# Optimization experiments

Measured on AMD Instinct MI355X. Metric: run time of the kernel, lower is better.

## Reference

```python
import jax, jax.numpy as jnp
import numpy as np

B, NQ, NK = 8, 1024, 1024
DQ = DK = DV = 512
H = 8
DH = DV // H
EPS = 1e-5
NEG = -1e9


def _layer_norm(x, g, b):
    mu = jnp.mean(x, axis=-1, keepdims=True)
    var = jnp.mean(jnp.square(x - mu), axis=-1, keepdims=True)
    return (x - mu) * jax.lax.rsqrt(var + EPS) * g + b


def setup_inputs() -> dict:
    key = jax.random.key(0)
    ks = jax.random.split(key, 16)
    s_q = 1.0 / np.sqrt(DQ)
    s_k = 1.0 / np.sqrt(DK)
    s_v = 1.0 / np.sqrt(DV)
    return {
        "Q": jax.random.normal(ks[0], (B, NQ, DQ), jnp.float32),
        "K": jax.random.normal(ks[1], (B, NK, DK), jnp.float32),
        "mask": jax.random.randint(ks[2], (B, NK), 0, 2, jnp.int32),
        "Wq": jax.random.uniform(ks[3], (DQ, DV), jnp.float32, -s_q, s_q),
        "bq": jax.random.uniform(ks[4], (DV,), jnp.float32, -s_q, s_q),
        "Wk": jax.random.uniform(ks[5], (DK, DV), jnp.float32, -s_k, s_k),
        "bk": jax.random.uniform(ks[6], (DV,), jnp.float32, -s_k, s_k),
        "Wv": jax.random.uniform(ks[7], (DK, DV), jnp.float32, -s_k, s_k),
        "bv": jax.random.uniform(ks[8], (DV,), jnp.float32, -s_k, s_k),
        "Wo": jax.random.uniform(ks[9], (DV, DV), jnp.float32, -s_v, s_v),
        "bo": jax.random.uniform(ks[10], (DV,), jnp.float32, -s_v, s_v),
        "g0": jnp.ones((DV,), jnp.float32),
        "b0": jnp.zeros((DV,), jnp.float32),
        "g1": jnp.ones((DV,), jnp.float32),
        "b1": jnp.zeros((DV,), jnp.float32),
    }


def reference(Q, K, mask, Wq, bq, Wk, bk, Wv, bv, Wo, bo, g0, b0, g1, b1):
    b = Q.shape[0]
    # projections: [B, N, DV] -> [B, N, H, DH]
    q = (Q @ Wq + bq).reshape(b, -1, H, DH)
    k = (K @ Wk + bk).reshape(b, -1, H, DH)
    v = (K @ Wv + bv).reshape(b, -1, H, DH)
    scores = jnp.einsum("bqhd,bkhd->bhqk", q, k) / np.sqrt(DH)  # [B,H,Nq,Nk]
    scores = jnp.where((mask == 0)[:, None, None, :], NEG, scores)
    A = jax.nn.softmax(scores, axis=-1)
    o = q + jnp.einsum("bhqk,bkhd->bqhd", A, v)  # residual on projected Q (per head)
    O = o.reshape(b, -1, DV)
    O = _layer_norm(O, g0, b0)
    O = O + jax.nn.relu(O @ Wo + bo)
    O = _layer_norm(O, g1, b1)
    return O
```

## Files before the change

### kernel.cpp

```cpp
#include <hip/hip_runtime.h>


typedef float f32x4 __attribute__((ext_vector_type(4)));
typedef short bf16x8 __attribute__((ext_vector_type(8)));
typedef unsigned short u16;

#define MFMA16 __builtin_amdgcn_mfma_f32_16x16x32_bf16

__device__ __forceinline__ float bf2f(u16 u){
    unsigned x = ((unsigned)u) << 16;
    return __builtin_bit_cast(float, x);
}
__device__ __forceinline__ u16 f2bf(float f){
    unsigned u = __builtin_bit_cast(unsigned, f);
    u = u + 0x7fffu + ((u >> 16) & 1u);
    return (u16)(u >> 16);
}

__global__ __launch_bounds__(256) void transpose_w(
    const float* __restrict__ Wq, const float* __restrict__ Wk,
    const float* __restrict__ Wv, const float* __restrict__ Wo,
    u16* __restrict__ wt)
{
    const int z = blockIdx.z;
    const float* W = (z == 0) ? Wq : (z == 1) ? Wk : (z == 2) ? Wv : Wo;
    u16* out = wt + (size_t)z * 512 * 512;

    __shared__ u16 tile[32][33];
    const int k0 = blockIdx.y * 32, n0 = blockIdx.x * 32;
    const int c = threadIdx.x & 31, r = threadIdx.x >> 5;
#pragma unroll
    for (int i = 0; i < 4; i++) {
        int rr = r + i * 8;
        tile[rr][c] = f2bf(W[(size_t)(k0 + rr) * 512 + n0 + c]);
    }
    __syncthreads();
#pragma unroll
    for (int i = 0; i < 4; i++) {
        int rr = r + i * 8;
        out[(size_t)(n0 + rr) * 512 + k0 + c] = tile[c][rr];
    }
}

__global__ __launch_bounds__(256) void transpose_v(
    const u16* __restrict__ vb, u16* __restrict__ vtg)
{
    __shared__ u16 tile[32][33];
    const int bh = blockIdx.z;
    const int b = bh >> 3, h = bh & 7;
    const int k0 = blockIdx.x * 32, d0 = blockIdx.y * 32;
    const int c = threadIdx.x & 31, r = threadIdx.x >> 5;
#pragma unroll
    for (int i = 0; i < 4; i++) {
        int rr = r + i * 8;
        tile[rr][c] = vb[(size_t)(b * 1024 + k0 + rr) * 512 + h * 64 + d0 + c];
    }
    __syncthreads();
#pragma unroll
    for (int i = 0; i < 4; i++) {
        int rr = r + i * 8;
        vtg[(size_t)(bh * 64 + d0 + rr) * 1024 + k0 + c] = tile[c][rr];
    }
}

__global__ __launch_bounds__(256) void gemm_proj(
    const float* __restrict__ Q, const float* __restrict__ K,
    const u16* __restrict__ wt,
    const float* __restrict__ bq, const float* __restrict__ bk, const float* __restrict__ bv,
    u16* __restrict__ qb, u16* __restrict__ kb, u16* __restrict__ vb)
{
    __shared__ __align__(16) u16 lds_a[128 * 40];
    __shared__ __align__(16) u16 lds_b[128 * 40];

    const int z = blockIdx.z;
    const float* X = (z == 0) ? Q : K;
    const u16* Wt = wt + (size_t)z * 512 * 512;
    const float* bias = (z == 0) ? bq : (z == 1) ? bk : bv;
    u16* outb = (z == 0) ? qb : (z == 1) ? kb : vb;

    const int bm = blockIdx.y, bn = blockIdx.x;
    const int t = threadIdx.x;
    const int wave = t >> 6, lane = t & 63, quad = lane >> 4, lm = lane & 15;
    const int wm = wave >> 1, wn = wave & 1;

    f32x4 acc[4][4];
    const f32x4 zz = {0.f, 0.f, 0.f, 0.f};
#pragma unroll
    for (int i = 0; i < 4; i++)
#pragma unroll
        for (int j = 0; j < 4; j++) acc[i][j] = zz;

    for (int k0 = 0; k0 < 512; k0 += 32) {
#pragma unroll
        for (int i = 0; i < 2; i++) {
            int idx = t + i * 256;
            int r = idx >> 2, c = (idx & 3) * 8;
            const float* xp = &X[(size_t)(bm * 128 + r) * 512 + k0 + c];
            f32x4 a0 = *(const f32x4*)xp;
            f32x4 a1 = *(const f32x4*)(xp + 4);
            bf16x8 xv;
#pragma unroll
            for (int j = 0; j < 4; j++) { xv[j] = (short)f2bf(a0[j]); xv[4 + j] = (short)f2bf(a1[j]); }
            *(bf16x8*)&lds_a[r * 40 + c] = xv;
            *(bf16x8*)&lds_b[r * 40 + c] =
                *(const bf16x8*)&Wt[(size_t)(bn * 128 + r) * 512 + k0 + c];
        }
        __syncthreads();
        bf16x8 af[4], bfr[4];
#pragma unroll
        for (int mi = 0; mi < 4; mi++)
            af[mi] = *(const bf16x8*)&lds_a[(wm * 64 + mi * 16 + lm) * 40 + quad * 8];
#pragma unroll
        for (int ni = 0; ni < 4; ni++)
            bfr[ni] = *(const bf16x8*)&lds_b[(wn * 64 + ni * 16 + lm) * 40 + quad * 8];
#pragma unroll
        for (int mi = 0; mi < 4; mi++)
#pragma unroll
            for (int ni = 0; ni < 4; ni++)
                acc[mi][ni] = MFMA16(af[mi], bfr[ni], acc[mi][ni], 0, 0, 0);
        __syncthreads();
    }

#pragma unroll
    for (int mi = 0; mi < 4; mi++) {
#pragma unroll
        for (int ni = 0; ni < 4; ni++) {
            const int col = bn * 128 + wn * 64 + ni * 16 + lm;
            const float bv_ = bias[col];
#pragma unroll
            for (int r = 0; r < 4; r++) {
                const int row = bm * 128 + wm * 64 + mi * 16 + quad * 4 + r;
                outb[(size_t)row * 512 + col] = f2bf(acc[mi][ni][r] + bv_);
            }
        }
    }
}

__global__ __launch_bounds__(256) void gemm_mlp(
    const u16* __restrict__ X, const u16* __restrict__ wt,
    const float* __restrict__ bo, const float* __restrict__ resid,
    float* __restrict__ outf)
{
    __shared__ __align__(16) u16 lds_a[128 * 40];
    __shared__ __align__(16) u16 lds_b[128 * 40];

    const u16* Wt = wt + (size_t)3 * 512 * 512;
    const int bm = blockIdx.y, bn = blockIdx.x;
    const int t = threadIdx.x;
    const int wave = t >> 6, lane = t & 63, quad = lane >> 4, lm = lane & 15;
    const int wm = wave >> 1, wn = wave & 1;

    f32x4 acc[4][4];
    const f32x4 zz = {0.f, 0.f, 0.f, 0.f};
#pragma unroll
    for (int i = 0; i < 4; i++)
#pragma unroll
        for (int j = 0; j < 4; j++) acc[i][j] = zz;

    for (int k0 = 0; k0 < 512; k0 += 32) {
#pragma unroll
        for (int i = 0; i < 2; i++) {
            int idx = t + i * 256;
            int r = idx >> 2, c = (idx & 3) * 8;
            *(bf16x8*)&lds_a[r * 40 + c] =
                *(const bf16x8*)&X[(size_t)(bm * 128 + r) * 512 + k0 + c];
            *(bf16x8*)&lds_b[r * 40 + c] =
                *(const bf16x8*)&Wt[(size_t)(bn * 128 + r) * 512 + k0 + c];
        }
        __syncthreads();
        bf16x8 af[4], bfr[4];
#pragma unroll
        for (int mi = 0; mi < 4; mi++)
            af[mi] = *(const bf16x8*)&lds_a[(wm * 64 + mi * 16 + lm) * 40 + quad * 8];
#pragma unroll
        for (int ni = 0; ni < 4; ni++)
            bfr[ni] = *(const bf16x8*)&lds_b[(wn * 64 + ni * 16 + lm) * 40 + quad * 8];
#pragma unroll
        for (int mi = 0; mi < 4; mi++)
#pragma unroll
            for (int ni = 0; ni < 4; ni++)
                acc[mi][ni] = MFMA16(af[mi], bfr[ni], acc[mi][ni], 0, 0, 0);
        __syncthreads();
    }

#pragma unroll
    for (int mi = 0; mi < 4; mi++) {
#pragma unroll
        for (int ni = 0; ni < 4; ni++) {
            const int col = bn * 128 + wn * 64 + ni * 16 + lm;
            const float bv_ = bo[col];
#pragma unroll
            for (int r = 0; r < 4; r++) {
                const int row = bm * 128 + wm * 64 + mi * 16 + quad * 4 + r;
                const size_t off = (size_t)row * 512 + col;
                outf[off] = resid[off] + fmaxf(acc[mi][ni][r] + bv_, 0.f);
            }
        }
    }
}

__global__ __launch_bounds__(256, 4) void attn_kernel(
    const u16* __restrict__ qb, const u16* __restrict__ kb, const u16* __restrict__ vtg,
    const int* __restrict__ mask, float* __restrict__ O)
{
    __shared__ __align__(16) u16 k_tile[64 * 88];
    __shared__ __align__(16) u16 vt[64 * 88];
    __shared__ __align__(16) u16 p_st[4 * 16 * 88];
    __shared__ float mbias[1024];

    const int i = blockIdx.x;
    const int s_ = i >> 3;
    const int bh = (i & 7) + 8 * (s_ >> 4);
    const int qt = s_ & 15;
    const int b = bh >> 3, h = bh & 7;

    const int t = threadIdx.x, wave = t >> 6, lane = t & 63;
    const int quad = lane >> 4, lm = lane & 15;
    const int qbase = qt * 64 + wave * 16;
    const size_t baseb = (size_t)b * 1024 * 512;
    const size_t vbase = (size_t)((b * 8 + h) * 64) * 1024;

#pragma unroll
    for (int ii = 0; ii < 4; ii++) {
        int j = t + ii * 256;
        mbias[j] = mask[b * 1024 + j] ? 0.0f : -30000.0f;
    }

    bf16x8 aq[2];
#pragma unroll
    for (int ks = 0; ks < 2; ks++)
        aq[ks] = *(const bf16x8*)&qb[baseb +
            (size_t)(qbase + lm) * 512 + h * 64 + ks * 32 + quad * 8];

    float lsum[4] = {0.f, 0.f, 0.f, 0.f};
    f32x4 oacc[4];
    const f32x4 zz = {0.f, 0.f, 0.f, 0.f};
#pragma unroll
    for (int c = 0; c < 4; c++) oacc[c] = zz;

    const float SC2 = 0.125f * 1.44269504088896341f;
    const int srow = t >> 2, scol = (t & 3) * 16;
    u16* pw = &p_st[wave * 16 * 88];

    const u16* kgp = &kb[baseb + (size_t)srow * 512 + h * 64 + scol];
    const u16* vgp = &vtg[vbase + (size_t)srow * 1024 + scol];

    bf16x8 kA0, kA1, vA0, vA1, kB0, kB1, vB0, vB1;

    auto load_t = [&](int kt, bf16x8& k0, bf16x8& k1, bf16x8& v0, bf16x8& v1) {
        const u16* kp = kgp + (size_t)kt * 64 * 512;
        k0 = *(const bf16x8*)kp;
        k1 = *(const bf16x8*)(kp + 8);
        const u16* vp = vgp + kt * 64;
        v0 = *(const bf16x8*)vp;
        v1 = *(const bf16x8*)(vp + 8);
    };
    auto store_t = [&](bf16x8 k0, bf16x8 k1, bf16x8 v0, bf16x8 v1) {
        *(bf16x8*)&k_tile[srow * 88 + scol]     = k0;
        *(bf16x8*)&k_tile[srow * 88 + scol + 8] = k1;
        *(bf16x8*)&vt[srow * 88 + scol]     = v0;
        *(bf16x8*)&vt[srow * 88 + scol + 8] = v1;
    };

    auto compute_t = [&](int kt) {
        const int keyg = kt * 64;
        bf16x8 bk[4][2];
#pragma unroll
        for (int n = 0; n < 4; n++)
#pragma unroll
            for (int ks = 0; ks < 2; ks++)
                bk[n][ks] = *(const bf16x8*)&k_tile[(n * 16 + lm) * 88 + ks * 32 + quad * 8];

#pragma unroll
        for (int n = 0; n < 4; n++) {
            f32x4 S = zz;
            __builtin_amdgcn_s_setprio(1);
            S = MFMA16(aq[0], bk[n][0], S, 0, 0, 0);
            S = MFMA16(aq[1], bk[n][1], S, 0, 0, 0);
            __builtin_amdgcn_s_setprio(0);
            const float bias = mbias[keyg + n * 16 + lm];
#pragma unroll
            for (int r = 0; r < 4; r++) {
                float p = __builtin_amdgcn_exp2f(__builtin_fmaf(S[r], SC2, bias));
                lsum[r] += p;
                pw[(quad * 4 + r) * 88 + n * 16 + lm] = f2bf(p);
            }
        }

#pragma unroll
        for (int ks = 0; ks < 2; ks++) {
            bf16x8 ap = *(const bf16x8*)&pw[lm * 88 + ks * 32 + quad * 8];
            __builtin_amdgcn_s_setprio(1);
#pragma unroll
            for (int c = 0; c < 4; c++) {
                bf16x8 bv_ = *(const bf16x8*)&vt[(c * 16 + lm) * 88 + ks * 32 + quad * 8];
                oacc[c] = MFMA16(ap, bv_, oacc[c], 0, 0, 0);
            }
            __builtin_amdgcn_s_setprio(0);
        }
    };

    load_t(0, kA0, kA1, vA0, vA1);

    for (int kt = 0; kt < 16; kt += 2) {
        store_t(kA0, kA1, vA0, vA1);
        load_t(kt + 1, kB0, kB1, vB0, vB1);
        __syncthreads();
        compute_t(kt);
        __syncthreads();
        store_t(kB0, kB1, vB0, vB1);
        load_t((kt + 2) & 15, kA0, kA1, vA0, vA1);
        __syncthreads();
        compute_t(kt + 1);
        __syncthreads();
    }

#pragma unroll
    for (int r = 0; r < 4; r++) {
        float s = lsum[r];
        s += __shfl_xor(s, 1); s += __shfl_xor(s, 2);
        s += __shfl_xor(s, 4); s += __shfl_xor(s, 8);
        lsum[r] = s;
    }

#pragma unroll
    for (int c = 0; c < 4; c++)
#pragma unroll
        for (int r = 0; r < 4; r++) {
            const int row = qbase + quad * 4 + r;
            const int d = h * 64 + c * 16 + lm;
            const size_t off = baseb + (size_t)row * 512 + d;
            O[off] = bf2f(qb[off]) + oacc[c][r] / lsum[r];
        }
}

__global__ __launch_bounds__(256) void ln_kernel(
    const float* __restrict__ in, const float* __restrict__ g, const float* __restrict__ bsh,
    u16* __restrict__ outb, float* __restrict__ outf)
{
    const int row = blockIdx.x * 4 + (threadIdx.x >> 6);
    const int lane = threadIdx.x & 63;
    const float* x = in + (size_t)row * 512 + lane * 8;
    float v[8];
    *(f32x4*)&v[0] = *(const f32x4*)&x[0];
    *(f32x4*)&v[4] = *(const f32x4*)&x[4];
    float s = 0.f, sq = 0.f;
#pragma unroll
    for (int j = 0; j < 8; j++) { s += v[j]; sq += v[j] * v[j]; }
#pragma unroll
    for (int off = 1; off < 64; off <<= 1) {
        s += __shfl_xor(s, off);
        sq += __shfl_xor(sq, off);
    }
    const float mu = s * (1.f / 512.f);
    const float var = sq * (1.f / 512.f) - mu * mu;
    const float rs = rsqrtf(var + 1e-5f);
    float y[8];
#pragma unroll
    for (int j = 0; j < 8; j++) {
        int col = lane * 8 + j;
        y[j] = (v[j] - mu) * rs * g[col] + bsh[col];
    }
    if (outb != nullptr) {
        bf16x8 ov;
#pragma unroll
        for (int j = 0; j < 8; j++) ov[j] = (short)f2bf(y[j]);
        *(bf16x8*)&outb[(size_t)row * 512 + lane * 8] = ov;
    }
    if (outf != nullptr) {
        float* o = outf + (size_t)row * 512 + lane * 8;
        *(f32x4*)&o[0] = *(const f32x4*)&y[0];
        *(f32x4*)&o[4] = *(const f32x4*)&y[4];
    }
}

extern "C" void kernel_launch(void* const* d_in, const int* in_sizes, int n_in,
                              void* d_out, int out_size, void* d_ws, size_t ws_size,
                              hipStream_t stream) {
    const float* Q  = (const float*)d_in[0];
    const float* K  = (const float*)d_in[1];
    const int* mask = (const int*)d_in[2];
    const float* Wq = (const float*)d_in[3];
    const float* bq = (const float*)d_in[4];
    const float* Wk = (const float*)d_in[5];
    const float* bk = (const float*)d_in[6];
    const float* Wv = (const float*)d_in[7];
    const float* bv = (const float*)d_in[8];
    const float* Wo = (const float*)d_in[9];
    const float* bo = (const float*)d_in[10];
    const float* g0 = (const float*)d_in[11];
    const float* b0 = (const float*)d_in[12];
    const float* g1 = (const float*)d_in[13];
    const float* b1 = (const float*)d_in[14];
    float* out = (float*)d_out;

    char* ws = (char*)d_ws;
    const size_t MB = 1048576;
    u16*   wt  = (u16*)(ws);
    u16*   qb  = (u16*)(ws + 2 * MB);
    u16*   kb  = (u16*)(ws + 10 * MB);
    u16*   vtg = (u16*)(ws + 18 * MB);
    u16*   vb  = (u16*)(ws + 26 * MB);
    float* Of  = (float*)(ws + 26 * MB);
    u16*   O1b = (u16*)(ws + 2 * MB);
    float* O1f = (float*)(ws + 10 * MB);
    float* Uf  = (float*)(ws + 26 * MB);

    transpose_w<<<dim3(16, 16, 4), 256, 0, stream>>>(Wq, Wk, Wv, Wo, wt);
    gemm_proj<<<dim3(4, 64, 3), 256, 0, stream>>>(Q, K, wt, bq, bk, bv, qb, kb, vb);
    transpose_v<<<dim3(32, 2, 64), 256, 0, stream>>>(vb, vtg);
    attn_kernel<<<1024, 256, 0, stream>>>(qb, kb, vtg, mask, Of);
    ln_kernel<<<2048, 256, 0, stream>>>(Of, g0, b0, O1b, O1f);
    gemm_mlp<<<dim3(4, 64, 1), 256, 0, stream>>>(O1b, wt, bo, O1f, Uf);
    ln_kernel<<<2048, 256, 0, stream>>>(Uf, g1, b1, nullptr, out);
}
```

Before: 207.4 us.

## Fuse V transpose into projection epilogue, pre-convert inputs, drop mask LDS staging

The V projection epilogue now writes its result straight into the per-head transposed layout, which removes the separate transpose_v kernel and its round trip through global memory. Q and K are converted to bf16 once in a new convert_x kernel, so the projection GEMM loads bf16 tiles instead of converting fp32 inside its inner loop. The attention kernel stops staging a mask-bias array in LDS and instead reads the mask from global memory on each key tile. In exchange this adds an extra kernel and extra bf16 buffers in the workspace, and the mask reads become repeated global loads.

```diff
diff --git a/kernel.cpp b/kernel.cpp
--- a/kernel.cpp
+++ b/kernel.cpp
@@ -4,6 +4,7 @@
 typedef float f32x4 __attribute__((ext_vector_type(4)));
 typedef short bf16x8 __attribute__((ext_vector_type(8)));
 typedef unsigned short u16;
+typedef unsigned short u16x4 __attribute__((ext_vector_type(4)));
 
 #define MFMA16 __builtin_amdgcn_mfma_f32_16x16x32_bf16
 
@@ -42,109 +43,36 @@
     }
 }
 
-__global__ __launch_bounds__(256) void transpose_v(
-    const u16* __restrict__ vb, u16* __restrict__ vtg)
-{
-    __shared__ u16 tile[32][33];
-    const int bh = blockIdx.z;
-    const int b = bh >> 3, h = bh & 7;
-    const int k0 = blockIdx.x * 32, d0 = blockIdx.y * 32;
-    const int c = threadIdx.x & 31, r = threadIdx.x >> 5;
-#pragma unroll
-    for (int i = 0; i < 4; i++) {
-        int rr = r + i * 8;
-        tile[rr][c] = vb[(size_t)(b * 1024 + k0 + rr) * 512 + h * 64 + d0 + c];
-    }
-    __syncthreads();
-#pragma unroll
-    for (int i = 0; i < 4; i++) {
-        int rr = r + i * 8;
-        vtg[(size_t)(bh * 64 + d0 + rr) * 1024 + k0 + c] = tile[c][rr];
-    }
+__global__ __launch_bounds__(256) void convert_x(
+    const float* __restrict__ Q, const float* __restrict__ K,
+    u16* __restrict__ xq, u16* __restrict__ xk)
+{
+    const float* src = blockIdx.y ? K : Q;
+    u16* dst = blockIdx.y ? xk : xq;
+    const size_t i = ((size_t)blockIdx.x * 256 + threadIdx.x) * 8;
+    f32x4 a0 = *(const f32x4*)&src[i];
+    f32x4 a1 = *(const f32x4*)&src[i + 4];
+    bf16x8 v;
+#pragma unroll
+    for (int j = 0; j < 4; j++) { v[j] = (short)f2bf(a0[j]); v[4 + j] = (short)f2bf(a1[j]); }
+    *(bf16x8*)&dst[i] = v;
 }
 
 __global__ __launch_bounds__(256) void gemm_proj(
-    const float* __restrict__ Q, const float* __restrict__ K,
+    const u16* __restrict__ xq, const u16* __restrict__ xk,
     const u16* __restrict__ wt,
     const float* __restrict__ bq, const float* __restrict__ bk, const float* __restrict__ bv,
-    u16* __restrict__ qb, u16* __restrict__ kb, u16* __restrict__ vb)
+    u16* __restrict__ qb, u16* __restrict__ kb, u16* __restrict__ vtg)
 {
     __shared__ __align__(16) u16 lds_a[128 * 40];
     __shared__ __align__(16) u16 lds_b[128 * 40];
 
     const int z = blockIdx.z;
-    const float* X = (z == 0) ? Q : K;
+    const u16* X = (z == 0) ? xq : xk;
     const u16* Wt = wt + (size_t)z * 512 * 512;
     const float* bias = (z == 0) ? bq : (z == 1) ? bk : bv;
-    u16* outb = (z == 0) ? qb : (z == 1) ? kb : vb;
-
-    const int bm = blockIdx.y, bn = blockIdx.x;
-    const int t = threadIdx.x;
-    const int wave = t >> 6, lane = t & 63, quad = lane >> 4, lm = lane & 15;
-    const int wm = wave >> 1, wn = wave & 1;
-
-    f32x4 acc[4][4];
-    const f32x4 zz = {0.f, 0.f, 0.f, 0.f};
-#pragma unroll
-    for (int i = 0; i < 4; i++)
-#pragma unroll
-        for (int j = 0; j < 4; j++) acc[i][j] = zz;
-
-    for (int k0 = 0; k0 < 512; k0 += 32) {
-#pragma unroll
-        for (int i = 0; i < 2; i++) {
-            int idx = t + i * 256;
-            int r = idx >> 2, c = (idx & 3) * 8;
-            const float* xp = &X[(size_t)(bm * 128 + r) * 512 + k0 + c];
-            f32x4 a0 = *(const f32x4*)xp;
-            f32x4 a1 = *(const f32x4*)(xp + 4);
-            bf16x8 xv;
-#pragma unroll
-            for (int j = 0; j < 4; j++) { xv[j] = (short)f2bf(a0[j]); xv[4 + j] = (short)f2bf(a1[j]); }
-            *(bf16x8*)&lds_a[r * 40 + c] = xv;
-            *(bf16x8*)&lds_b[r * 40 + c] =
-                *(const bf16x8*)&Wt[(size_t)(bn * 128 + r) * 512 + k0 + c];
-        }
-        __syncthreads();
-        bf16x8 af[4], bfr[4];
-#pragma unroll
-        for (int mi = 0; mi < 4; mi++)
-            af[mi] = *(const bf16x8*)&lds_a[(wm * 64 + mi * 16 + lm) * 40 + quad * 8];
-#pragma unroll
-        for (int ni = 0; ni < 4; ni++)
-            bfr[ni] = *(const bf16x8*)&lds_b[(wn * 64 + ni * 16 + lm) * 40 + quad * 8];
-#pragma unroll
-        for (int mi = 0; mi < 4; mi++)
-#pragma unroll
-            for (int ni = 0; ni < 4; ni++)
-                acc[mi][ni] = MFMA16(af[mi], bfr[ni], acc[mi][ni], 0, 0, 0);
-        __syncthreads();
-    }
-
-#pragma unroll
-    for (int mi = 0; mi < 4; mi++) {
-#pragma unroll
-        for (int ni = 0; ni < 4; ni++) {
-            const int col = bn * 128 + wn * 64 + ni * 16 + lm;
-            const float bv_ = bias[col];
-#pragma unroll
-            for (int r = 0; r < 4; r++) {
-                const int row = bm * 128 + wm * 64 + mi * 16 + quad * 4 + r;
-                outb[(size_t)row * 512 + col] = f2bf(acc[mi][ni][r] + bv_);
-            }
-        }
-    }
-}
-
-__global__ __launch_bounds__(256) void gemm_mlp(
-    const u16* __restrict__ X, const u16* __restrict__ wt,
-    const float* __restrict__ bo, const float* __restrict__ resid,
-    float* __restrict__ outf)
-{
-    __shared__ __align__(16) u16 lds_a[128 * 40];
-    __shared__ __align__(16) u16 lds_b[128 * 40];
-
-    const u16* Wt = wt + (size_t)3 * 512 * 512;
+    u16* outb = (z == 0) ? qb : kb;
+
     const int bm = blockIdx.y, bn = blockIdx.x;
     const int t = threadIdx.x;
     const int wave = t >> 6, lane = t & 63, quad = lane >> 4, lm = lane & 15;
@@ -183,6 +111,86 @@
         __syncthreads();
     }
 
+    if (z == 2) {
+#pragma unroll
+        for (int mi = 0; mi < 4; mi++) {
+            const int key0 = bm * 128 + wm * 64 + mi * 16 + quad * 4;
+            const int bb = key0 >> 10, key = key0 & 1023;
+#pragma unroll
+            for (int ni = 0; ni < 4; ni++) {
+                const int col = bn * 128 + wn * 64 + ni * 16 + lm;
+                const float bv_ = bias[col];
+                const int hh = col >> 6, dd = col & 63;
+                u16x4 pk;
+#pragma unroll
+                for (int r = 0; r < 4; r++) pk[r] = f2bf(acc[mi][ni][r] + bv_);
+                *(u16x4*)&vtg[((size_t)((bb * 8 + hh) * 64 + dd)) * 1024 + key] = pk;
+            }
+        }
+    } else {
+#pragma unroll
+        for (int mi = 0; mi < 4; mi++) {
+#pragma unroll
+            for (int ni = 0; ni < 4; ni++) {
+                const int col = bn * 128 + wn * 64 + ni * 16 + lm;
+                const float bv_ = bias[col];
+#pragma unroll
+                for (int r = 0; r < 4; r++) {
+                    const int row = bm * 128 + wm * 64 + mi * 16 + quad * 4 + r;
+                    outb[(size_t)row * 512 + col] = f2bf(acc[mi][ni][r] + bv_);
+                }
+            }
+        }
+    }
+}
+
+__global__ __launch_bounds__(256) void gemm_mlp(
+    const u16* __restrict__ X, const u16* __restrict__ wt,
+    const float* __restrict__ bo, const float* __restrict__ resid,
+    float* __restrict__ outf)
+{
+    __shared__ __align__(16) u16 lds_a[128 * 40];
+    __shared__ __align__(16) u16 lds_b[128 * 40];
+
+    const u16* Wt = wt + (size_t)3 * 512 * 512;
+    const int bm = blockIdx.y, bn = blockIdx.x;
+    const int t = threadIdx.x;
+    const int wave = t >> 6, lane = t & 63, quad = lane >> 4, lm = lane & 15;
+    const int wm = wave >> 1, wn = wave & 1;
+
+    f32x4 acc[4][4];
+    const f32x4 zz = {0.f, 0.f, 0.f, 0.f};
+#pragma unroll
+    for (int i = 0; i < 4; i++)
+#pragma unroll
+        for (int j = 0; j < 4; j++) acc[i][j] = zz;
+
+    for (int k0 = 0; k0 < 512; k0 += 32) {
+#pragma unroll
+        for (int i = 0; i < 2; i++) {
+            int idx = t + i * 256;
+            int r = idx >> 2, c = (idx & 3) * 8;
+            *(bf16x8*)&lds_a[r * 40 + c] =
+                *(const bf16x8*)&X[(size_t)(bm * 128 + r) * 512 + k0 + c];
+            *(bf16x8*)&lds_b[r * 40 + c] =
+                *(const bf16x8*)&Wt[(size_t)(bn * 128 + r) * 512 + k0 + c];
+        }
+        __syncthreads();
+        bf16x8 af[4], bfr[4];
+#pragma unroll
+        for (int mi = 0; mi < 4; mi++)
+            af[mi] = *(const bf16x8*)&lds_a[(wm * 64 + mi * 16 + lm) * 40 + quad * 8];
+#pragma unroll
+        for (int ni = 0; ni < 4; ni++)
+            bfr[ni] = *(const bf16x8*)&lds_b[(wn * 64 + ni * 16 + lm) * 40 + quad * 8];
+#pragma unroll
+        for (int mi = 0; mi < 4; mi++)
+#pragma unroll
+            for (int ni = 0; ni < 4; ni++)
+                acc[mi][ni] = MFMA16(af[mi], bfr[ni], acc[mi][ni], 0, 0, 0);
+        __syncthreads();
+    }
+
 #pragma unroll
     for (int mi = 0; mi < 4; mi++) {
 #pragma unroll
@@ -206,7 +214,6 @@
     __shared__ __align__(16) u16 k_tile[64 * 88];
     __shared__ __align__(16) u16 vt[64 * 88];
     __shared__ __align__(16) u16 p_st[4 * 16 * 88];
-    __shared__ float mbias[1024];
 
     const int i = blockIdx.x;
     const int s_ = i >> 3;
@@ -219,12 +226,7 @@
     const int qbase = qt * 64 + wave * 16;
     const size_t baseb = (size_t)b * 1024 * 512;
     const size_t vbase = (size_t)((b * 8 + h) * 64) * 1024;
-
-#pragma unroll
-    for (int ii = 0; ii < 4; ii++) {
-        int j = t + ii * 256;
-        mbias[j] = mask[b * 1024 + j] ? 0.0f : -30000.0f;
-    }
+    const int* mrow = &mask[b * 1024];
 
     bf16x8 aq[2];
 #pragma unroll
@@ -264,6 +266,11 @@
 
     auto compute_t = [&](int kt) {
         const int keyg = kt * 64;
+        float bias_n[4];
+#pragma unroll
+        for (int n = 0; n < 4; n++)
+            bias_n[n] = mrow[keyg + n * 16 + lm] ? 0.0f : -30000.0f;
+
         bf16x8 bk[4][2];
 #pragma unroll
         for (int n = 0; n < 4; n++)
@@ -278,10 +285,9 @@
             S = MFMA16(aq[0], bk[n][0], S, 0, 0, 0);
             S = MFMA16(aq[1], bk[n][1], S, 0, 0, 0);
             __builtin_amdgcn_s_setprio(0);
-            const float bias = mbias[keyg + n * 16 + lm];
 #pragma unroll
             for (int r = 0; r < 4; r++) {
-                float p = __builtin_amdgcn_exp2f(__builtin_fmaf(S[r], SC2, bias));
+                float p = __builtin_amdgcn_exp2f(__builtin_fmaf(S[r], SC2, bias_n[n]));
                 lsum[r] += p;
                 pw[(quad * 4 + r) * 88 + n * 16 + lm] = f2bf(p);
             }
@@ -400,15 +406,16 @@
     u16*   qb  = (u16*)(ws + 2 * MB);
     u16*   kb  = (u16*)(ws + 10 * MB);
     u16*   vtg = (u16*)(ws + 18 * MB);
-    u16*   vb  = (u16*)(ws + 26 * MB);
+    u16*   xq  = (u16*)(ws + 26 * MB);
+    u16*   xk  = (u16*)(ws + 34 * MB);
     float* Of  = (float*)(ws + 26 * MB);
     u16*   O1b = (u16*)(ws + 2 * MB);
     float* O1f = (float*)(ws + 10 * MB);
     float* Uf  = (float*)(ws + 26 * MB);
 
     transpose_w<<<dim3(16, 16, 4), 256, 0, stream>>>(Wq, Wk, Wv, Wo, wt);
-    gemm_proj<<<dim3(4, 64, 3), 256, 0, stream>>>(Q, K, wt, bq, bk, bv, qb, kb, vb);
-    transpose_v<<<dim3(32, 2, 64), 256, 0, stream>>>(vb, vtg);
+    convert_x<<<dim3(2048, 2), 256, 0, stream>>>(Q, K, xq, xk);
+    gemm_proj<<<dim3(4, 64, 3), 256, 0, stream>>>(xq, xk, wt, bq, bk, bv, qb, kb, vtg);
     attn_kernel<<<1024, 256, 0, stream>>>(qb, kb, vtg, mask, Of);
     ln_kernel<<<2048, 256, 0, stream>>>(Of, g0, b0, O1b, O1f);
     gemm_mlp<<<dim3(4, 64, 1), 256, 0, stream>>>(O1b, wt, bo, O1f, Uf);
```

Result: slower. 214.0 us (+3.2%).

## Keep softmax probabilities in registers via permlane swaps instead of LDS staging

Applied to the files above, without the earlier changes.

Computes S transposed (K as the A operand) so each lane holds four consecutive keys for one query. The bf16 probabilities are packed and rearranged into the PV MFMA A-operand layout with permlane32/permlane16 swaps, which removes the per-wave LDS staging buffer. The mask bias is now read straight from global memory as int4 vectors rather than precomputed into shared memory, and the row-sum reduction is rewritten for the new layout. This cuts LDS traffic and shared memory use, possibly raising occupancy, but relies on gfx950 permlane swap instructions and adds global mask loads inside the loop.

```diff
diff --git a/kernel.cpp b/kernel.cpp
--- a/kernel.cpp
+++ b/kernel.cpp
@@ -4,6 +4,10 @@
 typedef float f32x4 __attribute__((ext_vector_type(4)));
 typedef short bf16x8 __attribute__((ext_vector_type(8)));
 typedef unsigned short u16;
+typedef unsigned int u32;
+typedef unsigned int u32x2 __attribute__((ext_vector_type(2)));
+typedef unsigned int u32x4 __attribute__((ext_vector_type(4)));
+typedef int i32x4 __attribute__((ext_vector_type(4)));
 
 #define MFMA16 __builtin_amdgcn_mfma_f32_16x16x32_bf16
 
@@ -15,6 +19,23 @@
     unsigned u = __builtin_bit_cast(unsigned, f);
     u = u + 0x7fffu + ((u >> 16) & 1u);
     return (u16)(u >> 16);
+}
+
+__device__ __forceinline__ void plane32_swap(u32& a, u32& b){
+#if __has_builtin(__builtin_amdgcn_permlane32_swap)
+    u32x2 r = __builtin_amdgcn_permlane32_swap(a, b, false, false);
+    a = r[0]; b = r[1];
+#else
+    asm volatile("v_permlane32_swap_b32 %0, %1" : "+v"(a), "+v"(b));
+#endif
+}
+__device__ __forceinline__ void plane16_swap(u32& a, u32& b){
+#if __has_builtin(__builtin_amdgcn_permlane16_swap)
+    u32x2 r = __builtin_amdgcn_permlane16_swap(a, b, false, false);
+    a = r[0]; b = r[1];
+#else
+    asm volatile("v_permlane16_swap_b32 %0, %1" : "+v"(a), "+v"(b));
+#endif
 }
 
 __global__ __launch_bounds__(256) void transpose_w(
@@ -205,8 +226,6 @@
 {
     __shared__ __align__(16) u16 k_tile[64 * 88];
     __shared__ __align__(16) u16 vt[64 * 88];
-    __shared__ __align__(16) u16 p_st[4 * 16 * 88];
-    __shared__ float mbias[1024];
 
     const int i = blockIdx.x;
     const int s_ = i >> 3;
@@ -219,12 +238,7 @@
     const int qbase = qt * 64 + wave * 16;
     const size_t baseb = (size_t)b * 1024 * 512;
     const size_t vbase = (size_t)((b * 8 + h) * 64) * 1024;
-
-#pragma unroll
-    for (int ii = 0; ii < 4; ii++) {
-        int j = t + ii * 256;
-        mbias[j] = mask[b * 1024 + j] ? 0.0f : -30000.0f;
-    }
+    const int* mrow = &mask[b * 1024];
 
     bf16x8 aq[2];
 #pragma unroll
@@ -232,7 +246,7 @@
         aq[ks] = *(const bf16x8*)&qb[baseb +
             (size_t)(qbase + lm) * 512 + h * 64 + ks * 32 + quad * 8];
 
-    float lsum[4] = {0.f, 0.f, 0.f, 0.f};
+    float lsum_loc = 0.f;
     f32x4 oacc[4];
     const f32x4 zz = {0.f, 0.f, 0.f, 0.f};
 #pragma unroll
@@ -240,7 +254,6 @@
 
     const float SC2 = 0.125f * 1.44269504088896341f;
     const int srow = t >> 2, scol = (t & 3) * 16;
-    u16* pw = &p_st[wave * 16 * 88];
 
     const u16* kgp = &kb[baseb + (size_t)srow * 512 + h * 64 + scol];
     const u16* vgp = &vtg[vbase + (size_t)srow * 1024 + scol];
@@ -271,25 +284,43 @@
             for (int ks = 0; ks < 2; ks++)
                 bk[n][ks] = *(const bf16x8*)&k_tile[(n * 16 + lm) * 88 + ks * 32 + quad * 8];
 
-#pragma unroll
-        for (int n = 0; n < 4; n++) {
-            f32x4 S = zz;
-            __builtin_amdgcn_s_setprio(1);
-            S = MFMA16(aq[0], bk[n][0], S, 0, 0, 0);
-            S = MFMA16(aq[1], bk[n][1], S, 0, 0, 0);
-            __builtin_amdgcn_s_setprio(0);
-            const float bias = mbias[keyg + n * 16 + lm];
-#pragma unroll
-            for (int r = 0; r < 4; r++) {
-                float p = __builtin_amdgcn_exp2f(__builtin_fmaf(S[r], SC2, bias));
-                lsum[r] += p;
-                pw[(quad * 4 + r) * 88 + n * 16 + lm] = f2bf(p);
+        u32 W[2][4];
+#pragma unroll
+        for (int half = 0; half < 2; half++) {
+            u32 cP[2][2];
+#pragma unroll
+            for (int j = 0; j < 2; j++) {
+                const int n = half * 2 + j;
+                f32x4 S = zz;
+                __builtin_amdgcn_s_setprio(1);
+                S = MFMA16(bk[n][0], aq[0], S, 0, 0, 0);
+                S = MFMA16(bk[n][1], aq[1], S, 0, 0, 0);
+                __builtin_amdgcn_s_setprio(0);
+                i32x4 m4 = *(const i32x4*)&mrow[keyg + n * 16 + quad * 4];
+                float pr[4];
+#pragma unroll
+                for (int r = 0; r < 4; r++) {
+                    pr[r] = __builtin_amdgcn_exp2f(
+                        __builtin_fmaf(S[r], SC2, m4[r] ? 0.0f : -30000.0f));
+                    lsum_loc += pr[r];
+                }
+                cP[j][0] = (u32)f2bf(pr[0]) | ((u32)f2bf(pr[1]) << 16);
+                cP[j][1] = (u32)f2bf(pr[2]) | ((u32)f2bf(pr[3]) << 16);
             }
+#pragma unroll
+            for (int tt = 0; tt < 2; tt++) {
+                u32 a = cP[0][tt], b = cP[1][tt];
+                plane32_swap(a, b);
+                plane16_swap(a, b);
+                W[half][tt]     = a;
+                W[half][2 + tt] = b;
+            }
         }
 
 #pragma unroll
         for (int ks = 0; ks < 2; ks++) {
-            bf16x8 ap = *(const bf16x8*)&pw[lm * 88 + ks * 32 + quad * 8];
+            u32x4 wv = {W[ks][0], W[ks][1], W[ks][2], W[ks][3]};
+            bf16x8 ap = __builtin_bit_cast(bf16x8, wv);
             __builtin_amdgcn_s_setprio(1);
 #pragma unroll
             for (int c = 0; c < 4; c++) {
@@ -315,13 +346,12 @@
         __syncthreads();
     }
 
-#pragma unroll
-    for (int r = 0; r < 4; r++) {
-        float s = lsum[r];
-        s += __shfl_xor(s, 1); s += __shfl_xor(s, 2);
-        s += __shfl_xor(s, 4); s += __shfl_xor(s, 8);
-        lsum[r] = s;
-    }
+    float s = lsum_loc;
+    s += __shfl_xor(s, 16);
+    s += __shfl_xor(s, 32);
+    float lr[4];
+#pragma unroll
+    for (int r = 0; r < 4; r++) lr[r] = __shfl(s, quad * 4 + r);
 
 #pragma unroll
     for (int c = 0; c < 4; c++)
@@ -330,7 +360,7 @@
             const int row = qbase + quad * 4 + r;
             const int d = h * 64 + c * 16 + lm;
             const size_t off = baseb + (size_t)row * 512 + d;
-            O[off] = bf2f(qb[off]) + oacc[c][r] / lsum[r];
+            O[off] = bf2f(qb[off]) + oacc[c][r] / lr[r];
         }
 }
 
```

New measurement: 206.0 us. No clear change (-0.7%).

## Pre-convert Q/K to bf16 in a separate kernel; read mask directly in attention

Applied to the files above, without the earlier changes.

Adds a convert_x kernel that casts Q and K from fp32 to bf16 once. gemm_proj then loads bf16 activations instead of converting fp32 on every tile load, which it previously repeated across the 4 column blocks and for both the K and V projections. The attention kernel drops its shared-memory mask-bias table and reads the mask from global memory for each key tile. The trade-offs are an extra kernel launch with an additional bf16 write and read pass, and more global mask loads in the attention inner loop. Workspace offsets are rearranged so xq and vtg share the same slot.

```diff
diff --git a/kernel.cpp b/kernel.cpp
--- a/kernel.cpp
+++ b/kernel.cpp
@@ -42,29 +42,23 @@
     }
 }
 
-__global__ __launch_bounds__(256) void transpose_v(
-    const u16* __restrict__ vb, u16* __restrict__ vtg)
-{
-    __shared__ u16 tile[32][33];
-    const int bh = blockIdx.z;
-    const int b = bh >> 3, h = bh & 7;
-    const int k0 = blockIdx.x * 32, d0 = blockIdx.y * 32;
-    const int c = threadIdx.x & 31, r = threadIdx.x >> 5;
-#pragma unroll
-    for (int i = 0; i < 4; i++) {
-        int rr = r + i * 8;
-        tile[rr][c] = vb[(size_t)(b * 1024 + k0 + rr) * 512 + h * 64 + d0 + c];
-    }
-    __syncthreads();
-#pragma unroll
-    for (int i = 0; i < 4; i++) {
-        int rr = r + i * 8;
-        vtg[(size_t)(bh * 64 + d0 + rr) * 1024 + k0 + c] = tile[c][rr];
-    }
+__global__ __launch_bounds__(256) void convert_x(
+    const float* __restrict__ Q, const float* __restrict__ K,
+    u16* __restrict__ xq, u16* __restrict__ xk)
+{
+    const float* src = blockIdx.y ? K : Q;
+    u16* dst = blockIdx.y ? xk : xq;
+    const size_t i = ((size_t)blockIdx.x * 256 + threadIdx.x) * 8;
+    f32x4 a0 = *(const f32x4*)&src[i];
+    f32x4 a1 = *(const f32x4*)&src[i + 4];
+    bf16x8 v;
+#pragma unroll
+    for (int j = 0; j < 4; j++) { v[j] = (short)f2bf(a0[j]); v[4 + j] = (short)f2bf(a1[j]); }
+    *(bf16x8*)&dst[i] = v;
 }
 
 __global__ __launch_bounds__(256) void gemm_proj(
-    const float* __restrict__ Q, const float* __restrict__ K,
+    const u16* __restrict__ xq, const u16* __restrict__ xk,
     const u16* __restrict__ wt,
     const float* __restrict__ bq, const float* __restrict__ bk, const float* __restrict__ bv,
     u16* __restrict__ qb, u16* __restrict__ kb, u16* __restrict__ vb)
@@ -73,78 +67,11 @@
     __shared__ __align__(16) u16 lds_b[128 * 40];
 
     const int z = blockIdx.z;
-    const float* X = (z == 0) ? Q : K;
+    const u16* X = (z == 0) ? xq : xk;
     const u16* Wt = wt + (size_t)z * 512 * 512;
     const float* bias = (z == 0) ? bq : (z == 1) ? bk : bv;
     u16* outb = (z == 0) ? qb : (z == 1) ? kb : vb;
 
-    const int bm = blockIdx.y, bn = blockIdx.x;
-    const int t = threadIdx.x;
-    const int wave = t >> 6, lane = t & 63, quad = lane >> 4, lm = lane & 15;
-    const int wm = wave >> 1, wn = wave & 1;
-
-    f32x4 acc[4][4];
-    const f32x4 zz = {0.f, 0.f, 0.f, 0.f};
-#pragma unroll
-    for (int i = 0; i < 4; i++)
-#pragma unroll
-        for (int j = 0; j < 4; j++) acc[i][j] = zz;
-
-    for (int k0 = 0; k0 < 512; k0 += 32) {
-#pragma unroll
-        for (int i = 0; i < 2; i++) {
-            int idx = t + i * 256;
-            int r = idx >> 2, c = (idx & 3) * 8;
-            const float* xp = &X[(size_t)(bm * 128 + r) * 512 + k0 + c];
-            f32x4 a0 = *(const f32x4*)xp;
-            f32x4 a1 = *(const f32x4*)(xp + 4);
-            bf16x8 xv;
-#pragma unroll
-            for (int j = 0; j < 4; j++) { xv[j] = (short)f2bf(a0[j]); xv[4 + j] = (short)f2bf(a1[j]); }
-            *(bf16x8*)&lds_a[r * 40 + c] = xv;
-            *(bf16x8*)&lds_b[r * 40 + c] =
-                *(const bf16x8*)&Wt[(size_t)(bn * 128 + r) * 512 + k0 + c];
-        }
-        __syncthreads();
-        bf16x8 af[4], bfr[4];
-#pragma unroll
-        for (int mi = 0; mi < 4; mi++)
-            af[mi] = *(const bf16x8*)&lds_a[(wm * 64 + mi * 16 + lm) * 40 + quad * 8];
-#pragma unroll
-        for (int ni = 0; ni < 4; ni++)
-            bfr[ni] = *(const bf16x8*)&lds_b[(wn * 64 + ni * 16 + lm) * 40 + quad * 8];
-#pragma unroll
-        for (int mi = 0; mi < 4; mi++)
-#pragma unroll
-            for (int ni = 0; ni < 4; ni++)
-                acc[mi][ni] = MFMA16(af[mi], bfr[ni], acc[mi][ni], 0, 0, 0);
-        __syncthreads();
-    }
-
-#pragma unroll
-    for (int mi = 0; mi < 4; mi++) {
-#pragma unroll
-        for (int ni = 0; ni < 4; ni++) {
-            const int col = bn * 128 + wn * 64 + ni * 16 + lm;
-            const float bv_ = bias[col];
-#pragma unroll
-            for (int r = 0; r < 4; r++) {
-                const int row = bm * 128 + wm * 64 + mi * 16 + quad * 4 + r;
-                outb[(size_t)row * 512 + col] = f2bf(acc[mi][ni][r] + bv_);
-            }
-        }
-    }
-}
-
-__global__ __launch_bounds__(256) void gemm_mlp(
-    const u16* __restrict__ X, const u16* __restrict__ wt,
-    const float* __restrict__ bo, const float* __restrict__ resid,
-    float* __restrict__ outf)
-{
-    __shared__ __align__(16) u16 lds_a[128 * 40];
-    __shared__ __align__(16) u16 lds_b[128 * 40];
-
-    const u16* Wt = wt + (size_t)3 * 512 * 512;
     const int bm = blockIdx.y, bn = blockIdx.x;
     const int t = threadIdx.x;
     const int wave = t >> 6, lane = t & 63, quad = lane >> 4, lm = lane & 15;
@@ -188,6 +115,89 @@
 #pragma unroll
         for (int ni = 0; ni < 4; ni++) {
             const int col = bn * 128 + wn * 64 + ni * 16 + lm;
+            const float bv_ = bias[col];
+#pragma unroll
+            for (int r = 0; r < 4; r++) {
+                const int row = bm * 128 + wm * 64 + mi * 16 + quad * 4 + r;
+                outb[(size_t)row * 512 + col] = f2bf(acc[mi][ni][r] + bv_);
+            }
+        }
+    }
+}
+
+__global__ __launch_bounds__(256) void transpose_v(
+    const u16* __restrict__ vb, u16* __restrict__ vtg)
+{
+    __shared__ u16 tile[32][33];
+    const int bh = blockIdx.z;
+    const int b = bh >> 3, h = bh & 7;
+    const int k0 = blockIdx.x * 32, d0 = blockIdx.y * 32;
+    const int c = threadIdx.x & 31, r = threadIdx.x >> 5;
+#pragma unroll
+    for (int i = 0; i < 4; i++) {
+        int rr = r + i * 8;
+        tile[rr][c] = vb[(size_t)(b * 1024 + k0 + rr) * 512 + h * 64 + d0 + c];
+    }
+    __syncthreads();
+#pragma unroll
+    for (int i = 0; i < 4; i++) {
+        int rr = r + i * 8;
+        vtg[(size_t)(bh * 64 + d0 + rr) * 1024 + k0 + c] = tile[c][rr];
+    }
+}
+
+__global__ __launch_bounds__(256) void gemm_mlp(
+    const u16* __restrict__ X, const u16* __restrict__ wt,
+    const float* __restrict__ bo, const float* __restrict__ resid,
+    float* __restrict__ outf)
+{
+    __shared__ __align__(16) u16 lds_a[128 * 40];
+    __shared__ __align__(16) u16 lds_b[128 * 40];
+
+    const u16* Wt = wt + (size_t)3 * 512 * 512;
+    const int bm = blockIdx.y, bn = blockIdx.x;
+    const int t = threadIdx.x;
+    const int wave = t >> 6, lane = t & 63, quad = lane >> 4, lm = lane & 15;
+    const int wm = wave >> 1, wn = wave & 1;
+
+    f32x4 acc[4][4];
+    const f32x4 zz = {0.f, 0.f, 0.f, 0.f};
+#pragma unroll
+    for (int i = 0; i < 4; i++)
+#pragma unroll
+        for (int j = 0; j < 4; j++) acc[i][j] = zz;
+
+    for (int k0 = 0; k0 < 512; k0 += 32) {
+#pragma unroll
+        for (int i = 0; i < 2; i++) {
+            int idx = t + i * 256;
+            int r = idx >> 2, c = (idx & 3) * 8;
+            *(bf16x8*)&lds_a[r * 40 + c] =
+                *(const bf16x8*)&X[(size_t)(bm * 128 + r) * 512 + k0 + c];
+            *(bf16x8*)&lds_b[r * 40 + c] =
+                *(const bf16x8*)&Wt[(size_t)(bn * 128 + r) * 512 + k0 + c];
+        }
+        __syncthreads();
+        bf16x8 af[4], bfr[4];
+#pragma unroll
+        for (int mi = 0; mi < 4; mi++)
+            af[mi] = *(const bf16x8*)&lds_a[(wm * 64 + mi * 16 + lm) * 40 + quad * 8];
+#pragma unroll
+        for (int ni = 0; ni < 4; ni++)
+            bfr[ni] = *(const bf16x8*)&lds_b[(wn * 64 + ni * 16 + lm) * 40 + quad * 8];
+#pragma unroll
+        for (int mi = 0; mi < 4; mi++)
+#pragma unroll
+            for (int ni = 0; ni < 4; ni++)
+                acc[mi][ni] = MFMA16(af[mi], bfr[ni], acc[mi][ni], 0, 0, 0);
+        __syncthreads();
+    }
+
+#pragma unroll
+    for (int mi = 0; mi < 4; mi++) {
+#pragma unroll
+        for (int ni = 0; ni < 4; ni++) {
+            const int col = bn * 128 + wn * 64 + ni * 16 + lm;
             const float bv_ = bo[col];
 #pragma unroll
             for (int r = 0; r < 4; r++) {
@@ -206,7 +216,6 @@
     __shared__ __align__(16) u16 k_tile[64 * 88];
     __shared__ __align__(16) u16 vt[64 * 88];
     __shared__ __align__(16) u16 p_st[4 * 16 * 88];
-    __shared__ float mbias[1024];
 
     const int i = blockIdx.x;
     const int s_ = i >> 3;
@@ -219,12 +228,7 @@
     const int qbase = qt * 64 + wave * 16;
     const size_t baseb = (size_t)b * 1024 * 512;
     const size_t vbase = (size_t)((b * 8 + h) * 64) * 1024;
-
-#pragma unroll
-    for (int ii = 0; ii < 4; ii++) {
-        int j = t + ii * 256;
-        mbias[j] = mask[b * 1024 + j] ? 0.0f : -30000.0f;
-    }
+    const int* mrow = &mask[b * 1024];
 
     bf16x8 aq[2];
 #pragma unroll
@@ -264,6 +268,11 @@
 
     auto compute_t = [&](int kt) {
         const int keyg = kt * 64;
+        float bias_n[4];
+#pragma unroll
+        for (int n = 0; n < 4; n++)
+            bias_n[n] = mrow[keyg + n * 16 + lm] ? 0.0f : -30000.0f;
+
         bf16x8 bk[4][2];
 #pragma unroll
         for (int n = 0; n < 4; n++)
@@ -278,10 +287,9 @@
             S = MFMA16(aq[0], bk[n][0], S, 0, 0, 0);
             S = MFMA16(aq[1], bk[n][1], S, 0, 0, 0);
             __builtin_amdgcn_s_setprio(0);
-            const float bias = mbias[keyg + n * 16 + lm];
 #pragma unroll
             for (int r = 0; r < 4; r++) {
-                float p = __builtin_amdgcn_exp2f(__builtin_fmaf(S[r], SC2, bias));
+                float p = __builtin_amdgcn_exp2f(__builtin_fmaf(S[r], SC2, bias_n[n]));
                 lsum[r] += p;
                 pw[(quad * 4 + r) * 88 + n * 16 + lm] = f2bf(p);
             }
@@ -399,15 +407,18 @@
     u16*   wt  = (u16*)(ws);
     u16*   qb  = (u16*)(ws + 2 * MB);
     u16*   kb  = (u16*)(ws + 10 * MB);
+    u16*   xq  = (u16*)(ws + 18 * MB);
     u16*   vtg = (u16*)(ws + 18 * MB);
-    u16*   vb  = (u16*)(ws + 26 * MB);
+    u16*   xk  = (u16*)(ws + 26 * MB);
+    u16*   vb  = (u16*)(ws + 34 * MB);
     float* Of  = (float*)(ws + 26 * MB);
     u16*   O1b = (u16*)(ws + 2 * MB);
     float* O1f = (float*)(ws + 10 * MB);
     float* Uf  = (float*)(ws + 26 * MB);
 
     transpose_w<<<dim3(16, 16, 4), 256, 0, stream>>>(Wq, Wk, Wv, Wo, wt);
-    gemm_proj<<<dim3(4, 64, 3), 256, 0, stream>>>(Q, K, wt, bq, bk, bv, qb, kb, vb);
+    convert_x<<<dim3(2048, 2), 256, 0, stream>>>(Q, K, xq, xk);
+    gemm_proj<<<dim3(4, 64, 3), 256, 0, stream>>>(xq, xk, wt, bq, bk, bv, qb, kb, vb);
     transpose_v<<<dim3(32, 2, 64), 256, 0, stream>>>(vb, vtg);
     attn_kernel<<<1024, 256, 0, stream>>>(qb, kb, vtg, mask, Of);
     ln_kernel<<<2048, 256, 0, stream>>>(Of, g0, b0, O1b, O1f);
```

Result: slower. 214.8 us (+3.6%).
